# Kernel optimization log

Measured on AMD Instinct MI355X. Metric: run time of the kernel, lower is better.

## Reference

```python
import jax, jax.numpy as jnp
import numpy as np

N_HEAD = 16
N_FEAT = 1024
D_K = N_FEAT // N_HEAD


def setup_inputs() -> dict:
    key = jax.random.key(0)
    ks = jax.random.split(key, 11)
    B, T1, T2 = 2, 2048, 2048
    s = 0.02
    return {
        "query": jax.random.normal(ks[0], (B, T1, N_FEAT), jnp.float32),
        "key_": jax.random.normal(ks[1], (B, T2, N_FEAT), jnp.float32),
        "value": jax.random.normal(ks[2], (B, T2, N_FEAT), jnp.float32),
        "mask": jnp.ones((B, T1, T2), jnp.int32),
        "Wq": jax.random.normal(ks[3], (N_FEAT, N_FEAT), jnp.float32) * s,
        "bq": jnp.zeros((N_FEAT,), jnp.float32),
        "Wk": jax.random.normal(ks[4], (N_FEAT, N_FEAT), jnp.float32) * s,
        "bk": jnp.zeros((N_FEAT,), jnp.float32),
        "Wv": jax.random.normal(ks[5], (N_FEAT, N_FEAT), jnp.float32) * s,
        "bv": jnp.zeros((N_FEAT,), jnp.float32),
        "Wo": jax.random.normal(ks[6], (N_FEAT, N_FEAT), jnp.float32) * s,
        "bo": jnp.zeros((N_FEAT,), jnp.float32),
    }


def reference(query, key_, value, mask, Wq, bq, Wk, bk, Wv, bv, Wo, bo):
    B = query.shape[0]
    # project and split heads: (B, T, F) -> (B, H, T, d_k)
    def heads(x, W, b):
        y = x @ W + b
        return y.reshape(B, -1, N_HEAD, D_K).transpose(0, 2, 1, 3)

    q = heads(query, Wq, bq)
    k = heads(key_, Wk, bk)
    v = heads(value, Wv, bv)

    scale = jnp.sqrt(jnp.asarray(D_K, jnp.float32))
    scores = jnp.einsum("bhqd,bhkd->bhqk", q, k) / scale  # (B,H,T1,T2)
    m = mask[:, None, :, :]  # (B,1,T1,T2)
    scores = jnp.where(m > 0, scores, jnp.asarray(-10000.0, scores.dtype))
    attn = jax.nn.softmax(scores, axis=-1)
    # dropout_rate = 0.0 / inference -> identity
    x = jnp.einsum("bhqk,bhkd->bhqd", attn, v)
    x = x.transpose(0, 2, 1, 3).reshape(B, -1, N_FEAT)
    return x @ Wo + bo
```

## Files before the change

### kernel.cpp

```cpp
#include <hip/hip_runtime.h>
#include <hip/hip_bf16.h>
#include <stdint.h>

typedef float  f32x4 __attribute__((ext_vector_type(4)));
typedef short  s16x8 __attribute__((ext_vector_type(8)));
typedef short  s16x4 __attribute__((ext_vector_type(4)));
typedef int    i32x4 __attribute__((ext_vector_type(4)));

#define DI __device__ __forceinline__

constexpr int Bb = 2, Tt = 2048, Ff = 1024, Hh = 16, Dk = 64;
constexpr int Mm = Bb * Tt;
constexpr float LOG2E = 1.44269504088896340736f;

DI ushort f2bf(float f) {
  unsigned u = __float_as_uint(f);
  unsigned r = (u + 0x7fffu + ((u >> 16) & 1u)) >> 16;
  return (ushort)r;
}

DI int cvt_pk_bf16(float lo, float hi) {
  __hip_bfloat162 t = __float22bfloat162_rn(make_float2(lo, hi));
  int w;
  __builtin_memcpy(&w, &t, 4);
  return w;
}

DI void gload16(const void* g, void* l) {
  __builtin_amdgcn_global_load_lds(
      (__attribute__((address_space(1))) void*)g,
      (__attribute__((address_space(3))) void*)l, 16, 0, 0);
}

DI void wait_vm4() { asm volatile("s_waitcnt vmcnt(4)" ::: "memory"); }
DI void wait_vm0() { asm volatile("s_waitcnt vmcnt(0)" ::: "memory"); }

__global__ __launch_bounds__(256) void cvt3_kernel(const float* __restrict__ s0, const float* __restrict__ s1,
                                                   const float* __restrict__ s2, ushort* __restrict__ d0,
                                                   ushort* __restrict__ d1, ushort* __restrict__ d2, int n8) {
  const float* src = blockIdx.y == 0 ? s0 : (blockIdx.y == 1 ? s1 : s2);
  ushort* dst = blockIdx.y == 0 ? d0 : (blockIdx.y == 1 ? d1 : d2);
  int i = blockIdx.x * 256 + threadIdx.x;
  if (i >= n8) return;
  const float4* s4 = (const float4*)src + (size_t)i * 2;
  float4 a = s4[0], b = s4[1];
  s16x8 o;
  o[0] = (short)f2bf(a.x); o[1] = (short)f2bf(a.y); o[2] = (short)f2bf(a.z); o[3] = (short)f2bf(a.w);
  o[4] = (short)f2bf(b.x); o[5] = (short)f2bf(b.y); o[6] = (short)f2bf(b.z); o[7] = (short)f2bf(b.w);
  *((s16x8*)dst + i) = o;
}

__global__ __launch_bounds__(256) void wtrans_kernel(const float* __restrict__ W0, const float* __restrict__ W1,
                                                     const float* __restrict__ W2, const float* __restrict__ W3,
                                                     ushort* __restrict__ Wt0, ushort* __restrict__ Wt1,
                                                     ushort* __restrict__ Wt2, ushort* __restrict__ Wt3) {
  const float* W; ushort* Wt;
  switch (blockIdx.z) {
    case 0: W = W0; Wt = Wt0; break;
    case 1: W = W1; Wt = Wt1; break;
    case 2: W = W2; Wt = Wt2; break;
    default: W = W3; Wt = Wt3; break;
  }
  __shared__ float tile[64][65];
  int k0 = blockIdx.y * 64, n0 = blockIdx.x * 64;
  int t = threadIdx.x, r = t >> 4, c4 = (t & 15) * 4;
#pragma unroll
  for (int i = 0; i < 4; i++) {
    int row = r + i * 16;
    const float4 v = *(const float4*)(W + (size_t)(k0 + row) * Ff + n0 + c4);
    tile[row][c4] = v.x; tile[row][c4 + 1] = v.y; tile[row][c4 + 2] = v.z; tile[row][c4 + 3] = v.w;
  }
  __syncthreads();
#pragma unroll
  for (int i = 0; i < 4; i++) {
    int n = r + i * 16;
    s16x4 o;
#pragma unroll
    for (int j = 0; j < 4; j++) o[j] = (short)f2bf(tile[c4 + j][n]);
    *(s16x4*)(Wt + (size_t)(n0 + n) * Ff + k0 + c4) = o;
  }
}

__global__ __launch_bounds__(256) void maskflag_kernel(const int* __restrict__ mask, int* __restrict__ flags) {
  int kb = blockIdx.x, qb = blockIdx.y, b = blockIdx.z;
  int t = threadIdx.x;
  __shared__ int s;
  if (t == 0) s = 1;
  __syncthreads();
  int ok = 1;
#pragma unroll
  for (int i = 0; i < 4; i++) {
    int row = qb * 64 + (t >> 4) + i * 16;
    const int4 v = *(const int4*)(mask + ((size_t)b * Tt + row) * Tt + kb * 64 + (t & 15) * 4);
    ok &= (v.x > 0) & (v.y > 0) & (v.z > 0) & (v.w > 0);
  }
  atomicAnd(&s, ok);
  __syncthreads();
  if (t == 0) flags[(b * 32 + qb) * 32 + kb] = s;
}

DI void gemm_core(const ushort* __restrict__ A, const ushort* __restrict__ Bt,
                  const float* __restrict__ bias, void* __restrict__ Cout, float scale, int mode,
                  int m0, int n0) {
  __shared__ ushort Ads[3][128 * 32];
  __shared__ ushort Bds[3][128 * 32];
  const int tid = threadIdx.x, lane = tid & 63, w = tid >> 6;
  const int wr = w >> 1, wc = w & 1;
  const int g = lane >> 4, ln = lane & 15;
  const int strow = tid >> 2;
  const int stc = (tid & 3) * 8;

  const ushort* Asrc0 = A + (size_t)(m0 + strow) * Ff + stc;
  const ushort* Asrc1 = A + (size_t)(m0 + 64 + strow) * Ff + stc;
  const ushort* Bsrc0 = Bt + (size_t)(n0 + strow) * Ff + stc;
  const ushort* Bsrc1 = Bt + (size_t)(n0 + 64 + strow) * Ff + stc;
  const int dst0 = strow * 32 + stc;
  const int dst1 = (64 + strow) * 32 + stc;

  f32x4 acc[4][4];
#pragma unroll
  for (int m = 0; m < 4; m++)
#pragma unroll
    for (int n = 0; n < 4; n++) acc[m][n] = (f32x4){0.f, 0.f, 0.f, 0.f};

  auto stage = [&](int t, int slot) {
    const int k0 = t * 32;
    gload16(Asrc0 + k0, Ads[slot] + dst0);
    gload16(Asrc1 + k0, Ads[slot] + dst1);
    gload16(Bsrc0 + k0, Bds[slot] + dst0);
    gload16(Bsrc1 + k0, Bds[slot] + dst1);
  };

  stage(0, 0);
  stage(1, 1);

  int rs = 0, ws = 2;
  for (int t = 0; t < 32; ++t) {
    if (t < 31) wait_vm4(); else wait_vm0();
    __builtin_amdgcn_s_barrier();
    __builtin_amdgcn_sched_barrier(0);
    if (t < 30) stage(t + 2, ws);
    const ushort* As = Ads[rs];
    const ushort* Bs = Bds[rs];
    s16x8 af[4], bf[4];
#pragma unroll
    for (int m = 0; m < 4; m++) af[m] = *(const s16x8*)(As + (wr * 64 + m * 16 + ln) * 32 + g * 8);
#pragma unroll
    for (int n = 0; n < 4; n++) bf[n] = *(const s16x8*)(Bs + (wc * 64 + n * 16 + ln) * 32 + g * 8);
    __builtin_amdgcn_s_setprio(1);
#pragma unroll
    for (int m = 0; m < 4; m++)
#pragma unroll
      for (int n = 0; n < 4; n++)
        acc[m][n] = __builtin_amdgcn_mfma_f32_16x16x32_bf16(af[m], bf[n], acc[m][n], 0, 0, 0);
    __builtin_amdgcn_s_setprio(0);
    rs = rs == 2 ? 0 : rs + 1;
    ws = ws == 2 ? 0 : ws + 1;
  }
#pragma unroll
  for (int m = 0; m < 4; m++) {
    const int r0 = m0 + wr * 64 + m * 16 + g * 4;
#pragma unroll
    for (int n = 0; n < 4; n++) {
      const int col = n0 + wc * 64 + n * 16 + ln;
      const float bv = bias[col];
      if (mode == 2) {
        const int bb = r0 >> 11, rb = r0 & 2047;
        const int x = rb & 63;
        const int pbase = (x & 0x20) | ((x & 0x0C) << 1) | ((x & 0x10) >> 2);
        s16x4 o4;
#pragma unroll
        for (int r = 0; r < 4; r++) o4[r] = (short)f2bf(acc[m][n][r] + bv);
        *(s16x4*)((ushort*)Cout + ((size_t)bb * Ff + col) * Tt + (rb & ~63) + pbase) = o4;
      } else {
#pragma unroll
        for (int r = 0; r < 4; r++) {
          const float val = (acc[m][n][r] + bv) * scale;
          if (mode == 1)
            ((ushort*)Cout)[(size_t)(r0 + r) * Ff + col] = f2bf(val);
          else
            ((float*)Cout)[(size_t)(r0 + r) * Ff + col] = val;
        }
      }
    }
  }
}

__global__ __launch_bounds__(256) void qkv_gemm_kernel(
    const ushort* __restrict__ Xq, const ushort* __restrict__ Xk, const ushort* __restrict__ Xv,
    const ushort* __restrict__ Wqt, const ushort* __restrict__ Wkt, const ushort* __restrict__ Wvt,
    const float* __restrict__ bq, const float* __restrict__ bk, const float* __restrict__ bv,
    ushort* __restrict__ Qb, ushort* __restrict__ Kb, ushort* __restrict__ Vpt) {
  const int lin = blockIdx.x + 8 * blockIdx.y + 256 * blockIdx.z;
  const int work = (lin & 7) * 96 + (lin >> 3);
  const int z = work >> 8;
  const int r = work & 255;
  const int m0 = (r >> 3) * 128, n0 = (r & 7) * 128;
  const ushort* A = z == 0 ? Xq : (z == 1 ? Xk : Xv);
  const ushort* Wt = z == 0 ? Wqt : (z == 1 ? Wkt : Wvt);
  const float* bias = z == 0 ? bq : (z == 1 ? bk : bv);
  void* C = z == 0 ? (void*)Qb : (z == 1 ? (void*)Kb : (void*)Vpt);
  const float scale = z == 0 ? 0.125f * LOG2E : 1.0f;
  gemm_core(A, Wt, bias, C, scale, z == 2 ? 2 : 1, m0, n0);
}

__global__ __launch_bounds__(256) void out_gemm_kernel(const ushort* __restrict__ AO,
                                                       const ushort* __restrict__ Wot,
                                                       const float* __restrict__ bo,
                                                       float* __restrict__ Out) {
  const int lin = blockIdx.x + 8 * blockIdx.y;
  const int work = (lin & 7) * 32 + (lin >> 3);
  const int m0 = (work >> 3) * 128, n0 = (work & 7) * 128;
  gemm_core(AO, Wot, bo, Out, 1.0f, 0, m0, n0);
}

__global__ __launch_bounds__(256) void flash_kernel(
    const ushort* __restrict__ Qb, const ushort* __restrict__ Kb, const ushort* __restrict__ Vpt,
    const int* __restrict__ flags, const int* __restrict__ mask, ushort* __restrict__ AO) {
  __shared__ ushort Ks[2][64 * 64];
  __shared__ ushort Vs[2][64 * 64];
  const int lin = blockIdx.x + 16 * (blockIdx.y + 16 * blockIdx.z);
  const int work = (lin & 7) * 64 + (lin >> 3);
  const int qb = work & 15, h = (work >> 4) & 15, b = work >> 8;
  const int tid = threadIdx.x, lane = tid & 63, w = tid >> 6;
  const int g = lane >> 4, ln = lane & 15;

  const ushort* Qg = Qb + ((size_t)b * Tt + qb * 128) * Ff + h * Dk;
  const ushort* Kg = Kb + ((size_t)b * Tt) * Ff + h * Dk;
  const ushort* Vg = Vpt + (size_t)(b * Ff + h * Dk) * Tt;

  const int srow = lane >> 3;
  const int swzch = ((lane & 7) ^ srow) * 8;

  const ushort* ksrc0 = Kg + (size_t)(w * 16 + srow) * Ff + swzch;
  const ushort* ksrc1 = ksrc0 + (size_t)8 * Ff;
  const ushort* vsrc0 = Vg + (size_t)(w * 16 + srow) * Tt + swzch;
  const ushort* vsrc1 = vsrc0 + (size_t)8 * Tt;

  s16x8 qf0[2], qf1[2];
  {
    const ushort* Qrow0 = Qg + (size_t)(w * 16 + ln) * Ff;
    const ushort* Qrow1 = Qrow0 + (size_t)64 * Ff;
    qf0[0] = *(const s16x8*)(Qrow0 + g * 8);
    qf0[1] = *(const s16x8*)(Qrow0 + 32 + g * 8);
    qf1[0] = *(const s16x8*)(Qrow1 + g * 8);
    qf1[1] = *(const s16x8*)(Qrow1 + 32 + g * 8);
  }
  const int* flagrow0 = flags + (b * 32 + qb * 2) * 32;
  const int f0 = (lane < 32) ? flagrow0[lane] : 1;
  const int f1 = (lane < 32) ? flagrow0[32 + lane] : 1;

  {
    const int r0 = w * 16;
    gload16(ksrc0, Ks[0] + r0 * 64);
    gload16(ksrc1, Ks[0] + (r0 + 8) * 64);
    gload16(vsrc0, Vs[0] + r0 * 64);
    gload16(vsrc1, Vs[0] + (r0 + 8) * 64);
    ksrc0 += (size_t)64 * Ff; ksrc1 += (size_t)64 * Ff;
    vsrc0 += 64; vsrc1 += 64;
  }
  __syncthreads();
  const unsigned long long bm0 = __ballot(f0 == 0);
  const unsigned long long bm1 = __ballot(f1 == 0);

  int loff[4][2];
#pragma unroll
  for (int i = 0; i < 4; i++)
#pragma unroll
    for (int c = 0; c < 2; c++) {
      const int row = i * 16 + ln;
      loff[i][c] = row * 128 + ((c * 64 + g * 16) ^ ((row & 7) << 4));
    }
  const char* Kbase = (const char*)&Ks[0][0];
  const char* Vbase = (const char*)&Vs[0][0];

  f32x4 l0v = (f32x4){0.f, 0.f, 0.f, 0.f}, l1v = (f32x4){0.f, 0.f, 0.f, 0.f};
  f32x4 o0[4], o1[4];
#pragma unroll
  for (int ds = 0; ds < 4; ds++) { o0[ds] = (f32x4){0.f, 0.f, 0.f, 0.f}; o1[ds] = (f32x4){0.f, 0.f, 0.f, 0.f}; }

  auto body = [&](int bsel, int kt) {
    if (kt + 1 < 32) {
      ushort* Kn = Ks[bsel ^ 1];
      ushort* Vn = Vs[bsel ^ 1];
      const int r0 = w * 16;
      gload16(ksrc0, Kn + r0 * 64);
      gload16(ksrc1, Kn + (r0 + 8) * 64);
      gload16(vsrc0, Vn + r0 * 64);
      gload16(vsrc1, Vn + (r0 + 8) * 64);
      ksrc0 += (size_t)64 * Ff; ksrc1 += (size_t)64 * Ff;
      vsrc0 += 64; vsrc1 += 64;
    }
    const char* Kc = Kbase + bsel * 8192;
    const char* Vc = Vbase + bsel * 8192;
    f32x4 sf0[4], sf1[4];
    __builtin_amdgcn_s_setprio(1);
#pragma unroll
    for (int ks = 0; ks < 4; ++ks) {
      f32x4 a0 = (f32x4){0.f, 0.f, 0.f, 0.f};
      f32x4 a1 = (f32x4){0.f, 0.f, 0.f, 0.f};
#pragma unroll
      for (int c = 0; c < 2; c++) {
        const s16x8 kf = *(const s16x8*)(Kc + loff[ks][c]);
        a0 = __builtin_amdgcn_mfma_f32_16x16x32_bf16(kf, qf0[c], a0, 0, 0, 0);
        a1 = __builtin_amdgcn_mfma_f32_16x16x32_bf16(kf, qf1[c], a1, 0, 0, 0);
      }
      sf0[ks] = a0; sf1[ks] = a1;
    }
    __builtin_amdgcn_s_setprio(0);
    if ((bm0 >> kt) & 1ull) {
      const int qg_ = qb * 128 + w * 16 + ln;
#pragma unroll
      for (int ks = 0; ks < 4; ++ks) {
        const int4 mv = *(const int4*)(mask + ((size_t)b * Tt + qg_) * Tt + kt * 64 + ks * 16 + g * 4);
        if (mv.x <= 0) sf0[ks][0] = -10000.f;
        if (mv.y <= 0) sf0[ks][1] = -10000.f;
        if (mv.z <= 0) sf0[ks][2] = -10000.f;
        if (mv.w <= 0) sf0[ks][3] = -10000.f;
      }
    }
    if ((bm1 >> kt) & 1ull) {
      const int qg_ = qb * 128 + 64 + w * 16 + ln;
#pragma unroll
      for (int ks = 0; ks < 4; ++ks) {
        const int4 mv = *(const int4*)(mask + ((size_t)b * Tt + qg_) * Tt + kt * 64 + ks * 16 + g * 4);
        if (mv.x <= 0) sf1[ks][0] = -10000.f;
        if (mv.y <= 0) sf1[ks][1] = -10000.f;
        if (mv.z <= 0) sf1[ks][2] = -10000.f;
        if (mv.w <= 0) sf1[ks][3] = -10000.f;
      }
    }
#pragma unroll
    for (int ks = 0; ks < 4; ++ks) {
#pragma unroll
      for (int r = 0; r < 4; ++r) {
        sf0[ks][r] = __builtin_amdgcn_exp2f(sf0[ks][r]);
        sf1[ks][r] = __builtin_amdgcn_exp2f(sf1[ks][r]);
      }
    }
    l0v += sf0[0] + sf0[1] + sf0[2] + sf0[3];
    l1v += sf1[0] + sf1[1] + sf1[2] + sf1[3];
    i32x4 paw0[2], paw1[2];
#pragma unroll
    for (int c = 0; c < 2; c++)
#pragma unroll
      for (int f = 0; f < 2; f++)
#pragma unroll
        for (int hh = 0; hh < 2; hh++) {
          paw0[c][f * 2 + hh] = cvt_pk_bf16(sf0[2 * c + f][2 * hh], sf0[2 * c + f][2 * hh + 1]);
          paw1[c][f * 2 + hh] = cvt_pk_bf16(sf1[2 * c + f][2 * hh], sf1[2 * c + f][2 * hh + 1]);
        }
    const s16x8 pa00 = __builtin_bit_cast(s16x8, paw0[0]);
    const s16x8 pa01 = __builtin_bit_cast(s16x8, paw0[1]);
    const s16x8 pa10 = __builtin_bit_cast(s16x8, paw1[0]);
    const s16x8 pa11 = __builtin_bit_cast(s16x8, paw1[1]);
    __builtin_amdgcn_s_setprio(1);
#pragma unroll
    for (int ds = 0; ds < 4; ++ds) {
#pragma unroll
      for (int c = 0; c < 2; ++c) {
        const s16x8 vf = *(const s16x8*)(Vc + loff[ds][c]);
        o0[ds] = __builtin_amdgcn_mfma_f32_16x16x32_bf16(c == 0 ? pa00 : pa01, vf, o0[ds], 0, 0, 0);
        o1[ds] = __builtin_amdgcn_mfma_f32_16x16x32_bf16(c == 0 ? pa10 : pa11, vf, o1[ds], 0, 0, 0);
      }
    }
    __builtin_amdgcn_s_setprio(0);
    __syncthreads();
  };

  for (int kt = 0; kt < 32; kt += 2) {
    body(0, kt);
    body(1, kt + 1);
  }

  float l0 = (l0v[0] + l0v[1]) + (l0v[2] + l0v[3]);
  float l1 = (l1v[0] + l1v[1]) + (l1v[2] + l1v[3]);
  l0 += __shfl_xor(l0, 16); l0 += __shfl_xor(l0, 32);
  l1 += __shfl_xor(l1, 16); l1 += __shfl_xor(l1, 32);
  float inv0[4], inv1[4];
#pragma unroll
  for (int r = 0; r < 4; ++r) {
    inv0[r] = 1.0f / __shfl(l0, g * 4 + r);
    inv1[r] = 1.0f / __shfl(l1, g * 4 + r);
  }
  ushort* AOg0 = AO + ((size_t)b * Tt + qb * 128 + w * 16) * Ff + h * Dk;
  ushort* AOg1 = AOg0 + (size_t)64 * Ff;
#pragma unroll
  for (int ds = 0; ds < 4; ++ds)
#pragma unroll
    for (int r = 0; r < 4; ++r) {
      AOg0[(size_t)(g * 4 + r) * Ff + ds * 16 + ln] = f2bf(o0[ds][r] * inv0[r]);
      AOg1[(size_t)(g * 4 + r) * Ff + ds * 16 + ln] = f2bf(o1[ds][r] * inv1[r]);
    }
}

extern "C" void kernel_launch(void* const* d_in, const int* in_sizes, int n_in,
                              void* d_out, int out_size, void* d_ws, size_t ws_size,
                              hipStream_t stream) {
  const float* query = (const float*)d_in[0];
  const float* key_  = (const float*)d_in[1];
  const float* value = (const float*)d_in[2];
  const int*   mask  = (const int*)d_in[3];
  const float* Wq = (const float*)d_in[4];  const float* bq = (const float*)d_in[5];
  const float* Wk = (const float*)d_in[6];  const float* bk = (const float*)d_in[7];
  const float* Wv = (const float*)d_in[8];  const float* bv = (const float*)d_in[9];
  const float* Wo = (const float*)d_in[10]; const float* bo = (const float*)d_in[11];
  float* Out = (float*)d_out;

  constexpr size_t SZ_X = (size_t)Mm * Ff * 2;
  constexpr size_t SZ_W = (size_t)Ff * Ff * 2;
  uintptr_t p = (uintptr_t)d_ws;
  auto alloc = [&](size_t sz) { void* r = (void*)p; p += (sz + 255) & ~(size_t)255; return r; };
  ushort* Xq = (ushort*)alloc(SZ_X);
  ushort* Xk = (ushort*)alloc(SZ_X);
  ushort* Xv = (ushort*)alloc(SZ_X);
  ushort* Wqt = (ushort*)alloc(SZ_W);
  ushort* Wkt = (ushort*)alloc(SZ_W);
  ushort* Wvt = (ushort*)alloc(SZ_W);
  ushort* Wot = (ushort*)alloc(SZ_W);
  ushort* Qp  = (ushort*)alloc(SZ_X);
  ushort* Kp  = (ushort*)alloc(SZ_X);
  ushort* Vpt = (ushort*)alloc(SZ_X);
  int* flags = (int*)alloc((size_t)Bb * 32 * 32 * 4);
  ushort* AO = Xq;

  const int n8 = Mm * Ff / 8;
  cvt3_kernel<<<dim3(2048, 3), 256, 0, stream>>>(query, key_, value, Xq, Xk, Xv, n8);
  wtrans_kernel<<<dim3(16, 16, 4), 256, 0, stream>>>(Wq, Wk, Wv, Wo, Wqt, Wkt, Wvt, Wot);
  maskflag_kernel<<<dim3(32, 32, 2), 256, 0, stream>>>(mask, flags);
  qkv_gemm_kernel<<<dim3(8, 32, 3), 256, 0, stream>>>(Xq, Xk, Xv, Wqt, Wkt, Wvt, bq, bk, bv, Qp, Kp, Vpt);
  flash_kernel<<<dim3(16, 16, 2), 256, 0, stream>>>(Qp, Kp, Vpt, flags, mask, AO);
  out_gemm_kernel<<<dim3(8, 32), 256, 0, stream>>>(AO, Wot, bo, Out);
}
```

Measured before the change: 137.9 us.

## Fuse prep kernels, quad-buffer flash K/V tiles, compute row sums via MFMA

```diff
diff --git a/kernel.cpp b/kernel.cpp
--- a/kernel.cpp
+++ b/kernel.cpp
@@ -35,68 +35,72 @@
 DI void wait_vm4() { asm volatile("s_waitcnt vmcnt(4)" ::: "memory"); }
 DI void wait_vm0() { asm volatile("s_waitcnt vmcnt(0)" ::: "memory"); }
 
-__global__ __launch_bounds__(256) void cvt3_kernel(const float* __restrict__ s0, const float* __restrict__ s1,
-                                                   const float* __restrict__ s2, ushort* __restrict__ d0,
-                                                   ushort* __restrict__ d1, ushort* __restrict__ d2, int n8) {
-  const float* src = blockIdx.y == 0 ? s0 : (blockIdx.y == 1 ? s1 : s2);
-  ushort* dst = blockIdx.y == 0 ? d0 : (blockIdx.y == 1 ? d1 : d2);
-  int i = blockIdx.x * 256 + threadIdx.x;
-  if (i >= n8) return;
-  const float4* s4 = (const float4*)src + (size_t)i * 2;
-  float4 a = s4[0], b = s4[1];
-  s16x8 o;
-  o[0] = (short)f2bf(a.x); o[1] = (short)f2bf(a.y); o[2] = (short)f2bf(a.z); o[3] = (short)f2bf(a.w);
-  o[4] = (short)f2bf(b.x); o[5] = (short)f2bf(b.y); o[6] = (short)f2bf(b.z); o[7] = (short)f2bf(b.w);
-  *((s16x8*)dst + i) = o;
-}
-
-__global__ __launch_bounds__(256) void wtrans_kernel(const float* __restrict__ W0, const float* __restrict__ W1,
-                                                     const float* __restrict__ W2, const float* __restrict__ W3,
-                                                     ushort* __restrict__ Wt0, ushort* __restrict__ Wt1,
-                                                     ushort* __restrict__ Wt2, ushort* __restrict__ Wt3) {
-  const float* W; ushort* Wt;
-  switch (blockIdx.z) {
-    case 0: W = W0; Wt = Wt0; break;
-    case 1: W = W1; Wt = Wt1; break;
-    case 2: W = W2; Wt = Wt2; break;
-    default: W = W3; Wt = Wt3; break;
-  }
-  __shared__ float tile[64][65];
-  int k0 = blockIdx.y * 64, n0 = blockIdx.x * 64;
-  int t = threadIdx.x, r = t >> 4, c4 = (t & 15) * 4;
-#pragma unroll
-  for (int i = 0; i < 4; i++) {
-    int row = r + i * 16;
-    const float4 v = *(const float4*)(W + (size_t)(k0 + row) * Ff + n0 + c4);
-    tile[row][c4] = v.x; tile[row][c4 + 1] = v.y; tile[row][c4 + 2] = v.z; tile[row][c4 + 3] = v.w;
-  }
-  __syncthreads();
-#pragma unroll
-  for (int i = 0; i < 4; i++) {
-    int n = r + i * 16;
-    s16x4 o;
-#pragma unroll
-    for (int j = 0; j < 4; j++) o[j] = (short)f2bf(tile[c4 + j][n]);
-    *(s16x4*)(Wt + (size_t)(n0 + n) * Ff + k0 + c4) = o;
-  }
-}
-
-__global__ __launch_bounds__(256) void maskflag_kernel(const int* __restrict__ mask, int* __restrict__ flags) {
-  int kb = blockIdx.x, qb = blockIdx.y, b = blockIdx.z;
-  int t = threadIdx.x;
-  __shared__ int s;
-  if (t == 0) s = 1;
-  __syncthreads();
-  int ok = 1;
-#pragma unroll
-  for (int i = 0; i < 4; i++) {
-    int row = qb * 64 + (t >> 4) + i * 16;
-    const int4 v = *(const int4*)(mask + ((size_t)b * Tt + row) * Tt + kb * 64 + (t & 15) * 4);
-    ok &= (v.x > 0) & (v.y > 0) & (v.z > 0) & (v.w > 0);
-  }
-  atomicAnd(&s, ok);
-  __syncthreads();
-  if (t == 0) flags[(b * 32 + qb) * 32 + kb] = s;
+__global__ __launch_bounds__(256) void prep_kernel(
+    const float* __restrict__ s0, const float* __restrict__ s1, const float* __restrict__ s2,
+    ushort* __restrict__ d0, ushort* __restrict__ d1, ushort* __restrict__ d2,
+    const float* __restrict__ W0, const float* __restrict__ W1,
+    const float* __restrict__ W2, const float* __restrict__ W3,
+    ushort* __restrict__ Wt0, ushort* __restrict__ Wt1,
+    ushort* __restrict__ Wt2, ushort* __restrict__ Wt3,
+    const int* __restrict__ mask, int* __restrict__ flags) {
+  const int bid = blockIdx.x;
+  const int t = threadIdx.x;
+  if (bid < 6144) {
+    const int z = bid >> 11, x = bid & 2047;
+    const float* src = z == 0 ? s0 : (z == 1 ? s1 : s2);
+    ushort* dst = z == 0 ? d0 : (z == 1 ? d1 : d2);
+    const int i = x * 256 + t;
+    const float4* s4 = (const float4*)src + (size_t)i * 2;
+    float4 a = s4[0], b = s4[1];
+    s16x8 o;
+    o[0] = (short)f2bf(a.x); o[1] = (short)f2bf(a.y); o[2] = (short)f2bf(a.z); o[3] = (short)f2bf(a.w);
+    o[4] = (short)f2bf(b.x); o[5] = (short)f2bf(b.y); o[6] = (short)f2bf(b.z); o[7] = (short)f2bf(b.w);
+    *((s16x8*)dst + i) = o;
+  } else if (bid < 7168) {
+    const int wb = bid - 6144;
+    const int z = wb >> 8, bx = wb & 15, by = (wb >> 4) & 15;
+    const float* W; ushort* Wt;
+    switch (z) {
+      case 0: W = W0; Wt = Wt0; break;
+      case 1: W = W1; Wt = Wt1; break;
+      case 2: W = W2; Wt = Wt2; break;
+      default: W = W3; Wt = Wt3; break;
+    }
+    __shared__ float tile[64][65];
+    const int k0 = by * 64, n0 = bx * 64;
+    const int r = t >> 4, c4 = (t & 15) * 4;
+#pragma unroll
+    for (int i = 0; i < 4; i++) {
+      const int row = r + i * 16;
+      const float4 v = *(const float4*)(W + (size_t)(k0 + row) * Ff + n0 + c4);
+      tile[row][c4] = v.x; tile[row][c4 + 1] = v.y; tile[row][c4 + 2] = v.z; tile[row][c4 + 3] = v.w;
+    }
+    __syncthreads();
+#pragma unroll
+    for (int i = 0; i < 4; i++) {
+      const int n = r + i * 16;
+      s16x4 o;
+#pragma unroll
+      for (int j = 0; j < 4; j++) o[j] = (short)f2bf(tile[c4 + j][n]);
+      *(s16x4*)(Wt + (size_t)(n0 + n) * Ff + k0 + c4) = o;
+    }
+  } else {
+    const int mb = bid - 7168;
+    const int kb = mb & 31, qb = (mb >> 5) & 31, bz = mb >> 10;
+    __shared__ int s;
+    if (t == 0) s = 1;
+    __syncthreads();
+    int ok = 1;
+#pragma unroll
+    for (int i = 0; i < 4; i++) {
+      const int row = qb * 64 + (t >> 4) + i * 16;
+      const int4 v = *(const int4*)(mask + ((size_t)bz * Tt + row) * Tt + kb * 64 + (t & 15) * 4);
+      ok &= (v.x > 0) & (v.y > 0) & (v.z > 0) & (v.w > 0);
+    }
+    atomicAnd(&s, ok);
+    __syncthreads();
+    if (t == 0) flags[(bz * 32 + qb) * 32 + kb] = s;
+  }
 }
 
 DI void gemm_core(const ushort* __restrict__ A, const ushort* __restrict__ Bt,
@@ -217,8 +221,8 @@
 __global__ __launch_bounds__(256) void flash_kernel(
     const ushort* __restrict__ Qb, const ushort* __restrict__ Kb, const ushort* __restrict__ Vpt,
     const int* __restrict__ flags, const int* __restrict__ mask, ushort* __restrict__ AO) {
-  __shared__ ushort Ks[2][64 * 64];
-  __shared__ ushort Vs[2][64 * 64];
+  __shared__ ushort Ks[4][64 * 64];
+  __shared__ ushort Vs[4][64 * 64];
   const int lin = blockIdx.x + 16 * (blockIdx.y + 16 * blockIdx.z);
   const int work = (lin & 7) * 64 + (lin >> 3);
   const int qb = work & 15, h = (work >> 4) & 15, b = work >> 8;
@@ -250,15 +254,22 @@
   const int f0 = (lane < 32) ? flagrow0[lane] : 1;
   const int f1 = (lane < 32) ? flagrow0[32 + lane] : 1;
 
-  {
+  auto stage2 = [&](ushort* Kd0, ushort* Vd0, ushort* Kd1, ushort* Vd1) {
     const int r0 = w * 16;
-    gload16(ksrc0, Ks[0] + r0 * 64);
-    gload16(ksrc1, Ks[0] + (r0 + 8) * 64);
-    gload16(vsrc0, Vs[0] + r0 * 64);
-    gload16(vsrc1, Vs[0] + (r0 + 8) * 64);
-    ksrc0 += (size_t)64 * Ff; ksrc1 += (size_t)64 * Ff;
-    vsrc0 += 64; vsrc1 += 64;
-  }
+    gload16(ksrc0, Kd0 + r0 * 64);
+    gload16(ksrc1, Kd0 + (r0 + 8) * 64);
+    gload16(vsrc0, Vd0 + r0 * 64);
+    gload16(vsrc1, Vd0 + (r0 + 8) * 64);
+    gload16(ksrc0 + (size_t)64 * Ff, Kd1 + r0 * 64);
+    gload16(ksrc1 + (size_t)64 * Ff, Kd1 + (r0 + 8) * 64);
+    gload16(vsrc0 + 64, Vd1 + r0 * 64);
+    gload16(vsrc1 + 64, Vd1 + (r0 + 8) * 64);
+    ksrc0 += (size_t)128 * Ff; ksrc1 += (size_t)128 * Ff;
+    vsrc0 += 128; vsrc1 += 128;
+  };
+
+  stage2(Ks[0], Vs[0], Ks[1], Vs[1]);
+  stage2(Ks[2], Vs[2], Ks[3], Vs[3]);
   __syncthreads();
   const unsigned long long bm0 = __ballot(f0 == 0);
   const unsigned long long bm1 = __ballot(f1 == 0);
@@ -274,25 +285,18 @@
   const char* Kbase = (const char*)&Ks[0][0];
   const char* Vbase = (const char*)&Vs[0][0];
 
-  f32x4 l0v = (f32x4){0.f, 0.f, 0.f, 0.f}, l1v = (f32x4){0.f, 0.f, 0.f, 0.f};
+  s16x8 onesf;
+#pragma unroll
+  for (int j = 0; j < 8; ++j) onesf[j] = (short)0x3F80;
+
+  f32x4 accl0 = (f32x4){0.f, 0.f, 0.f, 0.f}, accl1 = (f32x4){0.f, 0.f, 0.f, 0.f};
   f32x4 o0[4], o1[4];
 #pragma unroll
   for (int ds = 0; ds < 4; ds++) { o0[ds] = (f32x4){0.f, 0.f, 0.f, 0.f}; o1[ds] = (f32x4){0.f, 0.f, 0.f, 0.f}; }
 
-  auto body = [&](int bsel, int kt) {
-    if (kt + 1 < 32) {
-      ushort* Kn = Ks[bsel ^ 1];
-      ushort* Vn = Vs[bsel ^ 1];
-      const int r0 = w * 16;
-      gload16(ksrc0, Kn + r0 * 64);
-      gload16(ksrc1, Kn + (r0 + 8) * 64);
-      gload16(vsrc0, Vn + r0 * 64);
-      gload16(vsrc1, Vn + (r0 + 8) * 64);
-      ksrc0 += (size_t)64 * Ff; ksrc1 += (size_t)64 * Ff;
-      vsrc0 += 64; vsrc1 += 64;
-    }
-    const char* Kc = Kbase + bsel * 8192;
-    const char* Vc = Vbase + bsel * 8192;
+  auto body = [&](int slot, int kt) {
+    const char* Kc = Kbase + slot * 8192;
+    const char* Vc = Vbase + slot * 8192;
     f32x4 sf0[4], sf1[4];
     __builtin_amdgcn_s_setprio(1);
 #pragma unroll
@@ -338,8 +342,6 @@
         sf1[ks][r] = __builtin_amdgcn_exp2f(sf1[ks][r]);
       }
     }
-    l0v += sf0[0] + sf0[1] + sf0[2] + sf0[3];
-    l1v += sf1[0] + sf1[1] + sf1[2] + sf1[3];
     i32x4 paw0[2], paw1[2];
 #pragma unroll
     for (int c = 0; c < 2; c++)
@@ -355,6 +357,10 @@
     const s16x8 pa10 = __builtin_bit_cast(s16x8, paw1[0]);
     const s16x8 pa11 = __builtin_bit_cast(s16x8, paw1[1]);
     __builtin_amdgcn_s_setprio(1);
+    accl0 = __builtin_amdgcn_mfma_f32_16x16x32_bf16(pa00, onesf, accl0, 0, 0, 0);
+    accl0 = __builtin_amdgcn_mfma_f32_16x16x32_bf16(pa01, onesf, accl0, 0, 0, 0);
+    accl1 = __builtin_amdgcn_mfma_f32_16x16x32_bf16(pa10, onesf, accl1, 0, 0, 0);
+    accl1 = __builtin_amdgcn_mfma_f32_16x16x32_bf16(pa11, onesf, accl1, 0, 0, 0);
 #pragma unroll
     for (int ds = 0; ds < 4; ++ds) {
 #pragma unroll
@@ -365,23 +371,24 @@
       }
     }
     __builtin_amdgcn_s_setprio(0);
-    __syncthreads();
   };
 
-  for (int kt = 0; kt < 32; kt += 2) {
+  for (int kt = 0; kt < 32; kt += 4) {
     body(0, kt);
     body(1, kt + 1);
-  }
-
-  float l0 = (l0v[0] + l0v[1]) + (l0v[2] + l0v[3]);
-  float l1 = (l1v[0] + l1v[1]) + (l1v[2] + l1v[3]);
-  l0 += __shfl_xor(l0, 16); l0 += __shfl_xor(l0, 32);
-  l1 += __shfl_xor(l1, 16); l1 += __shfl_xor(l1, 32);
+    __syncthreads();
+    if (kt + 4 < 32) stage2(Ks[0], Vs[0], Ks[1], Vs[1]);
+    body(2, kt + 2);
+    body(3, kt + 3);
+    __syncthreads();
+    if (kt + 6 < 32) stage2(Ks[2], Vs[2], Ks[3], Vs[3]);
+  }
+
   float inv0[4], inv1[4];
 #pragma unroll
   for (int r = 0; r < 4; ++r) {
-    inv0[r] = 1.0f / __shfl(l0, g * 4 + r);
-    inv1[r] = 1.0f / __shfl(l1, g * 4 + r);
+    inv0[r] = 1.0f / accl0[r];
+    inv1[r] = 1.0f / accl1[r];
   }
   ushort* AOg0 = AO + ((size_t)b * Tt + qb * 128 + w * 16) * Ff + h * Dk;
   ushort* AOg1 = AOg0 + (size_t)64 * Ff;
@@ -424,10 +431,9 @@
   int* flags = (int*)alloc((size_t)Bb * 32 * 32 * 4);
   ushort* AO = Xq;
 
-  const int n8 = Mm * Ff / 8;
-  cvt3_kernel<<<dim3(2048, 3), 256, 0, stream>>>(query, key_, value, Xq, Xk, Xv, n8);
-  wtrans_kernel<<<dim3(16, 16, 4), 256, 0, stream>>>(Wq, Wk, Wv, Wo, Wqt, Wkt, Wvt, Wot);
-  maskflag_kernel<<<dim3(32, 32, 2), 256, 0, stream>>>(mask, flags);
+  prep_kernel<<<dim3(9216), 256, 0, stream>>>(query, key_, value, Xq, Xk, Xv,
+                                              Wq, Wk, Wv, Wo, Wqt, Wkt, Wvt, Wot,
+                                              mask, flags);
   qkv_gemm_kernel<<<dim3(8, 32, 3), 256, 0, stream>>>(Xq, Xk, Xv, Wqt, Wkt, Wvt, bq, bk, bv, Qp, Kp, Vpt);
   flash_kernel<<<dim3(16, 16, 2), 256, 0, stream>>>(Qp, Kp, Vpt, flags, mask, AO);
   out_gemm_kernel<<<dim3(8, 32), 256, 0, stream>>>(AO, Wot, bo, Out);
```

Measured after the change: 132.6 us. 1.04x faster.
